# Performance work log

Hardware: AMD Instinct MI355X
Metric: run time of the kernel (lower is better)

The kernel has to match this reference:

```python
import jax, jax.numpy as jnp
import numpy as np
import math

B, N, T, H, HEADS, FIN, NL_TR = 4, 256, 16, 128, 4, 2, 5
M = B * N
NEG = -1e9

def _sinusoidal(t, h):
    pos = jnp.arange(t, dtype=jnp.float32)[:, None]
    div = jnp.exp(jnp.arange(0, h, 2, dtype=jnp.float32) * (-math.log(10000.0) / h))
    pe = jnp.zeros((t, h), dtype=jnp.float32)
    pe = pe.at[:, 0::2].set(jnp.sin(pos * div))
    pe = pe.at[:, 1::2].set(jnp.cos(pos * div))
    return pe

def _gat(x, W, a_src, a_dst, b, E, m):
    # x: [T,M,F]; W: [F,heads,H]; E: [T,M,M] bool, E[t,i,j]=edge j->i; m: [T,M] bool
    h = jnp.einsum('tmf,fhd->tmhd', x, W)
    ss = jnp.einsum('tmhd,hd->tmh', h, a_src)  # source score per node
    sd = jnp.einsum('tmhd,hd->tmh', h, a_dst)  # dest score per node
    logits = jax.nn.leaky_relu(sd[:, :, None, :] + ss[:, None, :, :], 0.2)  # [T,i,j,h]
    logits = jnp.where(E[..., None], logits, NEG)
    alpha = jax.nn.softmax(logits, axis=2)  # segment-softmax over incoming edges
    out = jnp.einsum('tijh,tjhd->tihd', alpha, h).mean(axis=2) + b  # concat=False -> head mean + bias
    return jax.nn.relu(out) * m[..., None]

def _ln(x, s, b):
    mu = x.mean(-1, keepdims=True)
    v = ((x - mu) ** 2).mean(-1, keepdims=True)
    return (x - mu) / jnp.sqrt(v + 1e-5) * s + b

def _forward(ego_mask, positions, adjacency, gat1_W, gat1_asrc, gat1_adst, gat1_b, gatW, gat_asrc, gat_adst, gat_b, Wqkv, bqkv, Wo, bo, ln1_s, ln1_b, ln2_s, ln2_b, Wff1, bff1, Wff2, bff2):
    m = jnp.transpose(ego_mask, (1, 0, 2)).reshape(T, M)  # [T, B*N]
    eye = jnp.eye(M, dtype=bool)
    # edge j->i valid iff A[t,j,i]!=0 and both nodes masked; PyG GATConv adds self-loops
    E = ((jnp.swapaxes(adjacency, 1, 2) != 0) & m[:, :, None] & m[:, None, :]) | (eye[None] & m[:, :, None])
    x = _gat(positions, gat1_W, gat1_asrc, gat1_adst, gat1_b, E, m)
    for i in range(5):
        x = _gat(x, gatW[i], gat_asrc[i], gat_adst[i], gat_b[i], E, m)
    x_seq = jnp.transpose(x, (1, 0, 2)) + _sinusoidal(T, H)[None]  # [M, T, H]
    dh = H // HEADS
    scale = 1.0 / math.sqrt(dh)
    for l in range(NL_TR):
        q = (x_seq @ Wqkv[l, 0] + bqkv[l, 0]).reshape(M, T, HEADS, dh)
        k = (x_seq @ Wqkv[l, 1] + bqkv[l, 1]).reshape(M, T, HEADS, dh)
        v = (x_seq @ Wqkv[l, 2] + bqkv[l, 2]).reshape(M, T, HEADS, dh)
        sc = jnp.einsum('bqhd,bkhd->bhqk', q, k) * scale
        a = jax.nn.softmax(sc, axis=-1)
        o = jnp.einsum('bhqk,bkhd->bqhd', a, v).reshape(M, T, H) @ Wo[l] + bo[l]
        x_seq = _ln(x_seq + o, ln1_s[l], ln1_b[l])
        f = jax.nn.relu(x_seq @ Wff1[l] + bff1[l]) @ Wff2[l] + bff2[l]
        x_seq = _ln(x_seq + f, ln2_s[l], ln2_b[l])
    return x_seq.reshape(B, N, T, H)

def setup_inputs() -> dict:
    key = jax.random.key(0)
    ks = jax.random.split(key, 32)
    s = 0.05
    f32 = jnp.float32
    inp = {
        'ego_mask': jax.random.uniform(ks[0], (B, T, N)) < 0.95,
        'positions': jax.random.normal(ks[1], (T, M, FIN), dtype=f32),
        'adjacency': (jax.random.uniform(ks[2], (T, M, M)) < 0.02).astype(f32),
        'gat1_W': jax.random.normal(ks[3], (FIN, HEADS, H), dtype=f32) * s,
        'gat1_asrc': jax.random.normal(ks[4], (HEADS, H), dtype=f32) * s,
        'gat1_adst': jax.random.normal(ks[5], (HEADS, H), dtype=f32) * s,
        'gat1_b': jnp.zeros((H,), dtype=f32),
        'gatW': jax.random.normal(ks[6], (5, H, HEADS, H), dtype=f32) * s,
        'gat_asrc': jax.random.normal(ks[7], (5, HEADS, H), dtype=f32) * s,
        'gat_adst': jax.random.normal(ks[8], (5, HEADS, H), dtype=f32) * s,
        'gat_b': jnp.zeros((5, H), dtype=f32),
        'Wqkv': jax.random.normal(ks[9], (NL_TR, 3, H, H), dtype=f32) * s,
        'bqkv': jnp.zeros((NL_TR, 3, H), dtype=f32),
        'Wo': jax.random.normal(ks[10], (NL_TR, H, H), dtype=f32) * s,
        'bo': jnp.zeros((NL_TR, H), dtype=f32),
        'ln1_s': jnp.ones((NL_TR, H), dtype=f32),
        'ln1_b': jnp.zeros((NL_TR, H), dtype=f32),
        'ln2_s': jnp.ones((NL_TR, H), dtype=f32),
        'ln2_b': jnp.zeros((NL_TR, H), dtype=f32),
        'Wff1': jax.random.normal(ks[11], (NL_TR, H, 4 * H), dtype=f32) * s,
        'bff1': jnp.zeros((NL_TR, 4 * H), dtype=f32),
        'Wff2': jax.random.normal(ks[12], (NL_TR, 4 * H, H), dtype=f32) * s,
        'bff2': jnp.zeros((NL_TR, H), dtype=f32),
    }
    return inp

def reference(ego_mask, positions, adjacency, gat1_W, gat1_asrc, gat1_adst, gat1_b, gatW, gat_asrc, gat_adst, gat_b, Wqkv, bqkv, Wo, bo, ln1_s, ln1_b, ln2_s, ln2_b, Wff1, bff1, Wff2, bff2):
    return _forward(ego_mask, positions, adjacency, gat1_W, gat1_asrc, gat1_adst, gat1_b, gatW, gat_asrc, gat_adst, gat_b, Wqkv, bqkv, Wo, bo, ln1_s, ln1_b, ln2_s, ln2_b, Wff1, bff1, Wff2, bff2)
```

## Files before the change

### kernel.cpp

```cpp
#include <hip/hip_runtime.h>
#include <hip/hip_bf16.h>

#define TT 16
#define MM 1024
#define HDIM 128
#define NHEADS 4
#define NROWS (TT*MM)
#define MAXDEG 64

typedef __bf16 bf16x8 __attribute__((ext_vector_type(8)));
typedef float f32x4 __attribute__((ext_vector_type(4)));

__device__ __forceinline__ unsigned short f2b(float x) {
    unsigned u = __float_as_uint(x);
    u += 0x7fff + ((u >> 16) & 1);
    return (unsigned short)(u >> 16);
}
__device__ __forceinline__ float bu2f(unsigned short u) {
    return __uint_as_float(((unsigned)u) << 16);
}

__global__ __launch_bounds__(256) void k_init(const int* __restrict__ ego,
                                              float* __restrict__ mfl,
                                              int* __restrict__ cnt) {
    int idx = blockIdx.x * 256 + threadIdx.x;
    int t = idx >> 10, i = idx & 1023;
    int b = i >> 8, n = i & 255;
    mfl[idx] = ego[b * (TT * 256) + t * 256 + n] ? 1.f : 0.f;
    cnt[idx] = 0;
}

__global__ __launch_bounds__(256) void k_edges(const float* __restrict__ adj,
                                               const float* __restrict__ mfl,
                                               int* __restrict__ cnt,
                                               int* __restrict__ nbr) {
    int bid = blockIdx.x;
    int t = bid >> 6, jc = bid & 63;
    int tid = threadIdx.x;
    int i0 = tid * 4;
    int rowb = t * MM;
    float mi[4];
#pragma unroll
    for (int r = 0; r < 4; ++r) mi[r] = mfl[rowb + i0 + r];
    __shared__ float ms[16];
    if (tid < 16) ms[tid] = mfl[rowb + jc * 16 + tid];
    __syncthreads();
    const float* at = adj + (size_t)t * MM * MM;
#pragma unroll 4
    for (int jj = 0; jj < 16; ++jj) {
        int j = jc * 16 + jj;
        float4 a = *(const float4*)(at + (size_t)j * MM + i0);
        float mj = ms[jj];
#pragma unroll
        for (int r = 0; r < 4; ++r) {
            int i = i0 + r;
            bool e;
            if (j == i) e = (mi[r] != 0.f);
            else e = ((&a.x)[r] != 0.f) && (mj != 0.f) && (mi[r] != 0.f);
            if (e) {
                int row = rowb + i;
                int pos = atomicAdd(&cnt[row], 1);
                if (pos < MAXDEG) nbr[(size_t)row * MAXDEG + pos] = j;
            }
        }
    }
}

__global__ __launch_bounds__(256) void k_prep(const float* __restrict__ Wqkv,
                                              const float* __restrict__ Wo,
                                              const float* __restrict__ Wff1,
                                              const float* __restrict__ Wff2,
                                              const float* __restrict__ gW,
                                              unsigned short* __restrict__ Wb) {
    int o = blockIdx.x * 256 + threadIdx.x;
    const float* src; int cs;
    if (o < 122880) {
        int l = o / 24576, r = o % 24576;
        if (r < 6144) {
            int nt = r >> 8, rem = r & 255, ks = rem >> 6, lane = rem & 63;
            int mt = nt >> 3, cc = nt & 7;
            int k = ks * 32 + ((lane >> 4) << 3), c = cc * 16 + (lane & 15);
            src = Wqkv + ((size_t)(l * 3 + mt) * 128 + k) * 128 + c; cs = 128;
        } else if (r < 8192) {
            int u = r - 6144, nt = u >> 8, rem = u & 255, ks = rem >> 6, lane = rem & 63;
            int k = ks * 32 + ((lane >> 4) << 3), c = nt * 16 + (lane & 15);
            src = Wo + (size_t)l * 16384 + (size_t)k * 128 + c; cs = 128;
        } else if (r < 16384) {
            int u = r - 8192, nt = u >> 8, rem = u & 255, ks = rem >> 6, lane = rem & 63;
            int k = ks * 32 + ((lane >> 4) << 3), c = nt * 16 + (lane & 15);
            src = Wff1 + (size_t)l * 65536 + (size_t)k * 512 + c; cs = 512;
        } else {
            int u = r - 16384, nt = u >> 10, rem = u & 1023, ks = rem >> 6, lane = rem & 63;
            int k = ks * 32 + ((lane >> 4) << 3), c = nt * 16 + (lane & 15);
            src = Wff2 + (size_t)l * 65536 + (size_t)k * 128 + c; cs = 128;
        }
    } else {
        int u = o - 122880;
        int l = u >> 13, rr = u & 8191;
        int nt = rr >> 8, rem = rr & 255, ks = rem >> 6, lane = rem & 63;
        int k = ks * 32 + ((lane >> 4) << 3), c = nt * 16 + (lane & 15);
        src = gW + (size_t)l * 65536 + (size_t)k * 512 + c; cs = 512;
    }
    unsigned v[4];
#pragma unroll
    for (int j = 0; j < 4; ++j)
        v[j] = (unsigned)f2b(src[(2 * j) * (size_t)cs]) |
               ((unsigned)f2b(src[(2 * j + 1) * (size_t)cs]) << 16);
    *(uint4*)(Wb + (size_t)o * 8) = make_uint4(v[0], v[1], v[2], v[3]);
}

__global__ __launch_bounds__(128) void k_gat1(const float* __restrict__ x,
                                              const float* __restrict__ W,
                                              const float* __restrict__ asrc,
                                              const float* __restrict__ adst,
                                              unsigned short* __restrict__ h16,
                                              float* __restrict__ ss,
                                              float* __restrict__ sd) {
    int bid = blockIdx.x;
    int row = ((bid & 7) << 11) + (bid >> 3);
    int tid = threadIdx.x;
    float x0 = x[row * 2], x1 = x[row * 2 + 1];
    float s4[4], d4[4];
#pragma unroll
    for (int hh = 0; hh < 4; ++hh) {
        int o = hh * 128 + tid;
        float v = x0 * W[o] + x1 * W[512 + o];
        h16[(size_t)row * 512 + o] = f2b(v);
        s4[hh] = v * asrc[o];
        d4[hh] = v * adst[o];
    }
#pragma unroll
    for (int hh = 0; hh < 4; ++hh)
        for (int off = 32; off; off >>= 1) {
            s4[hh] += __shfl_down(s4[hh], off, 64);
            d4[hh] += __shfl_down(d4[hh], off, 64);
        }
    __shared__ float red[2][2][4];
    if ((tid & 63) == 0) {
        int w = tid >> 6;
#pragma unroll
        for (int hh = 0; hh < 4; ++hh) { red[w][0][hh] = s4[hh]; red[w][1][hh] = d4[hh]; }
    }
    __syncthreads();
    if (tid < 4) ss[row * 4 + tid] = red[0][0][tid] + red[1][0][tid];
    else if (tid < 8) sd[row * 4 + tid - 4] = red[0][1][tid - 4] + red[1][1][tid - 4];
}

__global__ __launch_bounds__(256, 2) void k_gat_h(const unsigned short* __restrict__ x16,
                                                  const unsigned short* __restrict__ Wg,
                                                  const float* __restrict__ asrc,
                                                  const float* __restrict__ adst,
                                                  unsigned short* __restrict__ h16,
                                                  float* __restrict__ ss,
                                                  float* __restrict__ sd) {
    __shared__ __align__(16) unsigned short xb[32 * 136];
    int bid = blockIdx.x;
    int row0 = (((bid & 7) << 6) + (bid >> 3)) * 32;
    int tid = threadIdx.x;
#pragma unroll
    for (int q = 0; q < 2; ++q) {
        int u = tid + q * 256;
        int rr = u >> 4, cc = (u & 15) * 8;
        *(uint4*)(xb + rr * 136 + cc) = *(const uint4*)(x16 + (size_t)(row0 + rr) * 128 + cc);
    }
    __syncthreads();
    const int lane = tid & 63, w = tid >> 6;
    const int mrow = lane & 15, quad = lane >> 4;
    float ps[2][4] = {{0,0,0,0},{0,0,0,0}}, pd[2][4] = {{0,0,0,0},{0,0,0,0}};
#pragma unroll
    for (int ib = 0; ib < 4; ++ib) {
        bf16x8 wb[8];
#pragma unroll
        for (int u = 0; u < 2; ++u) {
            int nt = w * 8 + ib * 2 + u;
#pragma unroll
            for (int ks = 0; ks < 4; ++ks)
                wb[u * 4 + ks] = *(const bf16x8*)(Wg + (size_t)((nt * 4 + ks) * 64 + lane) * 8);
        }
#pragma unroll
        for (int rg = 0; rg < 2; ++rg) {
            bf16x8 af[4];
#pragma unroll
            for (int ks = 0; ks < 4; ++ks)
                af[ks] = *(const bf16x8*)(xb + (rg * 16 + mrow) * 136 + ks * 32 + quad * 8);
            f32x4 acc[2];
            acc[0] = (f32x4){0.f, 0.f, 0.f, 0.f};
            acc[1] = (f32x4){0.f, 0.f, 0.f, 0.f};
#pragma unroll
            for (int u = 0; u < 2; ++u)
#pragma unroll
                for (int ks = 0; ks < 4; ++ks)
                    acc[u] = __builtin_amdgcn_mfma_f32_16x16x32_bf16(af[ks], wb[u * 4 + ks], acc[u], 0, 0, 0);
#pragma unroll
            for (int u = 0; u < 2; ++u) {
                int nt = w * 8 + ib * 2 + u, col = nt * 16 + mrow;
                float as_ = asrc[col], ad_ = adst[col];
#pragma unroll
                for (int r = 0; r < 4; ++r) {
                    float v = acc[u][r];
                    h16[(size_t)(row0 + rg * 16 + quad * 4 + r) * 512 + col] = f2b(v);
                    ps[rg][r] += v * as_; pd[rg][r] += v * ad_;
                }
            }
        }
    }
#pragma unroll
    for (int off = 1; off < 16; off <<= 1)
#pragma unroll
        for (int rg = 0; rg < 2; ++rg)
#pragma unroll
            for (int r = 0; r < 4; ++r) {
                ps[rg][r] += __shfl_xor(ps[rg][r], off, 64);
                pd[rg][r] += __shfl_xor(pd[rg][r], off, 64);
            }
    if (mrow == 0) {
#pragma unroll
        for (int rg = 0; rg < 2; ++rg)
#pragma unroll
            for (int r = 0; r < 4; ++r) {
                int row = row0 + rg * 16 + quad * 4 + r;
                ss[row * 4 + w] = ps[rg][r];
                sd[row * 4 + w] = pd[rg][r];
            }
    }
}

__global__ __launch_bounds__(256, 2) void k_agg(const unsigned short* __restrict__ h16,
                                                const float* __restrict__ ss,
                                                const float* __restrict__ sd,
                                                const int* __restrict__ cnt,
                                                const int* __restrict__ nbr,
                                                const float* __restrict__ mfl,
                                                const float* __restrict__ bias,
                                                unsigned short* __restrict__ xo16) {
    __shared__ float alB[4][MAXDEG][4];
    __shared__ int   nbB[4][MAXDEG];
    __shared__ __align__(16) float partB[4][512];
    int bid = blockIdx.x;
    int row0 = (((bid & 7) << 9) + (bid >> 3)) * 4;
    int tid = threadIdx.x;
    const int w = tid >> 6, lane = tid & 63;
    int row = row0 + w, t = row >> 10;
    bool valid = mfl[row] != 0.f;
    int c = 0;
    if (valid) { c = cnt[row]; if (c > MAXDEG) c = MAXDEG; }
    bool act = lane < c;
    int jreg = 0;
    float lg[4];
    if (act) {
        jreg = nbr[(size_t)row * MAXDEG + lane];
        int jr = t * MM + jreg;
#pragma unroll
        for (int hh = 0; hh < 4; ++hh) {
            float v = sd[row * 4 + hh] + ss[jr * 4 + hh];
            lg[hh] = v > 0.f ? v : 0.2f * v;
        }
    } else {
#pragma unroll
        for (int hh = 0; hh < 4; ++hh) lg[hh] = -1e30f;
    }
    float mx[4];
#pragma unroll
    for (int hh = 0; hh < 4; ++hh) mx[hh] = lg[hh];
#pragma unroll
    for (int off = 32; off; off >>= 1)
#pragma unroll
        for (int hh = 0; hh < 4; ++hh) mx[hh] = fmaxf(mx[hh], __shfl_xor(mx[hh], off, 64));
    float ev[4];
#pragma unroll
    for (int hh = 0; hh < 4; ++hh) ev[hh] = act ? __expf(lg[hh] - mx[hh]) : 0.f;
    float sm[4];
#pragma unroll
    for (int hh = 0; hh < 4; ++hh) sm[hh] = ev[hh];
#pragma unroll
    for (int off = 32; off; off >>= 1)
#pragma unroll
        for (int hh = 0; hh < 4; ++hh) sm[hh] += __shfl_xor(sm[hh], off, 64);
    if (act) {
        float4 a4 = make_float4(ev[0] / sm[0], ev[1] / sm[1], ev[2] / sm[2], ev[3] / sm[3]);
        *(float4*)&alB[w][lane][0] = a4;
        nbB[w][lane] = jreg;
    }
    __syncthreads();
    const int head = lane >> 4;
    float acc[8] = {0, 0, 0, 0, 0, 0, 0, 0};
    const unsigned short* hb = h16 + (size_t)t * MM * 512 + lane * 8;
    for (int n = 0; n < c; ++n) {
        int j = nbB[w][n];
        float a = alB[w][n][head];
        uint4 v = *(const uint4*)(hb + (size_t)j * 512);
        acc[0] += a * bu2f((unsigned short)(v.x & 0xffff));
        acc[1] += a * bu2f((unsigned short)(v.x >> 16));
        acc[2] += a * bu2f((unsigned short)(v.y & 0xffff));
        acc[3] += a * bu2f((unsigned short)(v.y >> 16));
        acc[4] += a * bu2f((unsigned short)(v.z & 0xffff));
        acc[5] += a * bu2f((unsigned short)(v.z >> 16));
        acc[6] += a * bu2f((unsigned short)(v.w & 0xffff));
        acc[7] += a * bu2f((unsigned short)(v.w >> 16));
    }
    *(float4*)&partB[w][lane * 8]     = make_float4(acc[0], acc[1], acc[2], acc[3]);
    *(float4*)&partB[w][lane * 8 + 4] = make_float4(acc[4], acc[5], acc[6], acc[7]);
    __syncthreads();
    {
        int d0 = lane * 2;
        unsigned outp = 0;
#pragma unroll
        for (int q = 0; q < 2; ++q) {
            int d = d0 + q;
            float v = 0.f;
            if (valid) {
                v = 0.25f * (partB[w][d] + partB[w][128 + d] + partB[w][256 + d] + partB[w][384 + d])
                    + bias[d];
                v = fmaxf(v, 0.f);
            }
            outp |= ((unsigned)f2b(v)) << (16 * q);
        }
        *(unsigned*)(xo16 + (size_t)row * 128 + d0) = outp;
    }
}

__device__ __forceinline__ void ln256(float* xs, const float* s, const float* b) {
    int tid = threadIdx.x, row = tid >> 4, lane = tid & 15;
    float* xr = xs + row * 128;
    float sum = 0.f;
#pragma unroll
    for (int k2 = 0; k2 < 8; ++k2) sum += xr[lane + 16 * k2];
#pragma unroll
    for (int off = 8; off; off >>= 1) sum += __shfl_xor(sum, off, 16);
    float mean = sum * (1.f / 128.f);
    float vs = 0.f;
#pragma unroll
    for (int k2 = 0; k2 < 8; ++k2) { float d = xr[lane + 16 * k2] - mean; vs += d * d; }
#pragma unroll
    for (int off = 8; off; off >>= 1) vs += __shfl_xor(vs, off, 16);
    float rstd = rsqrtf(vs * (1.f / 128.f) + 1e-5f);
#pragma unroll
    for (int k2 = 0; k2 < 8; ++k2) {
        int d = lane + 16 * k2;
        float v = (xr[d] - mean) * rstd;
        xr[d] = v * s[d] + b[d];
    }
    __syncthreads();
}

__global__ __launch_bounds__(256, 2) void k_tf(const unsigned short* __restrict__ xg,
        const unsigned short* __restrict__ Wb,
        const float* __restrict__ bqkv, const float* __restrict__ bo,
        const float* __restrict__ ln1s, const float* __restrict__ ln1b,
        const float* __restrict__ ln2s, const float* __restrict__ ln2b,
        const float* __restrict__ bff1, const float* __restrict__ bff2,
        float* __restrict__ out) {
    __shared__ __align__(16) float smem[8320];
    float* xs = smem;
    float* sb = smem + 2048;
    unsigned short* xb16  = (unsigned short*)(smem + 3072);
    unsigned short* Qb16  = (unsigned short*)(smem + 4160);
    unsigned short* Kb16  = (unsigned short*)(smem + 5248);
    unsigned short* Vb16  = (unsigned short*)(smem + 6336);
    unsigned short* hid16 = (unsigned short*)(smem + 4160);
    const int m = blockIdx.x, tid = threadIdx.x;
    const int lane = tid & 63, w = tid >> 6;
    const int mrow = lane & 15, quad = lane >> 4;

    for (int idx = tid; idx < 2048; idx += 256) {
        int t = idx >> 7, d = idx & 127, jj = d >> 1;
        float arg = (float)t * expf(-(float)(2 * jj) * (9.210340371976184f / 128.f));
        float pe = (d & 1) ? cosf(arg) : sinf(arg);
        xs[idx] = bu2f(xg[(size_t)t * (MM * HDIM) + (size_t)m * HDIM + d]) + pe;
    }
    __syncthreads();

    const int crow = tid >> 4, ccb = (tid & 15) * 8;
    for (int l = 0; l < 5; ++l) {
        const unsigned short* Wl = Wb + (size_t)l * 196608;
        {
            const float* xp = xs + crow * 128 + ccb;
            unsigned v[4];
#pragma unroll
            for (int j = 0; j < 4; ++j)
                v[j] = (unsigned)f2b(xp[2 * j]) | ((unsigned)f2b(xp[2 * j + 1]) << 16);
            *(uint4*)(xb16 + crow * 136 + ccb) = make_uint4(v[0], v[1], v[2], v[3]);
        }
        __syncthreads();
        {
            bf16x8 af[4];
#pragma unroll
            for (int ks = 0; ks < 4; ++ks)
                af[ks] = *(const bf16x8*)(xb16 + mrow * 136 + ks * 32 + quad * 8);
            f32x4 acc[6];
#pragma unroll
            for (int i = 0; i < 6; ++i) acc[i] = (f32x4){0.f, 0.f, 0.f, 0.f};
#pragma unroll
            for (int ib = 0; ib < 3; ++ib) {
                bf16x8 wb[8];
#pragma unroll
                for (int u = 0; u < 2; ++u) {
                    int nt = w * 6 + ib * 2 + u;
                    const unsigned short* bp = Wl + (size_t)(nt * 4) * 512 + lane * 8;
#pragma unroll
                    for (int ks = 0; ks < 4; ++ks)
                        wb[u * 4 + ks] = *(const bf16x8*)(bp + ks * 512);
                }
#pragma unroll
                for (int u = 0; u < 2; ++u)
#pragma unroll
                    for (int ks = 0; ks < 4; ++ks)
                        acc[ib * 2 + u] = __builtin_amdgcn_mfma_f32_16x16x32_bf16(af[ks], wb[u * 4 + ks], acc[ib * 2 + u], 0, 0, 0);
            }
#pragma unroll
            for (int i = 0; i < 6; ++i) {
                int nt = w * 6 + i, mt = nt >> 3, cc = nt & 7;
                int col = cc * 16 + mrow;
                float bb = bqkv[l * 384 + mt * 128 + col];
                unsigned short* dst = (mt == 0) ? Qb16 : (mt == 1) ? Kb16 : Vb16;
#pragma unroll
                for (int r = 0; r < 4; ++r)
                    dst[(quad * 4 + r) * 136 + col] = f2b(acc[i][r] + bb);
            }
        }
        __syncthreads();
        {
            int hh = tid >> 6, tq = (tid >> 2) & 15, tk0 = (tid & 3) * 4;
            const unsigned short* qp = Qb16 + tq * 136 + hh * 32;
            float a[4] = {0.f, 0.f, 0.f, 0.f};
#pragma unroll
            for (int d4 = 0; d4 < 4; ++d4) {
                uint4 qv = *(const uint4*)(qp + d4 * 8);
                float qf[8];
                qf[0] = bu2f((unsigned short)(qv.x & 0xffff)); qf[1] = bu2f((unsigned short)(qv.x >> 16));
                qf[2] = bu2f((unsigned short)(qv.y & 0xffff)); qf[3] = bu2f((unsigned short)(qv.y >> 16));
                qf[4] = bu2f((unsigned short)(qv.z & 0xffff)); qf[5] = bu2f((unsigned short)(qv.z >> 16));
                qf[6] = bu2f((unsigned short)(qv.w & 0xffff)); qf[7] = bu2f((unsigned short)(qv.w >> 16));
#pragma unroll
                for (int j = 0; j < 4; ++j) {
                    uint4 kv = *(const uint4*)(Kb16 + (tk0 + j) * 136 + hh * 32 + d4 * 8);
                    a[j] += qf[0] * bu2f((unsigned short)(kv.x & 0xffff));
                    a[j] += qf[1] * bu2f((unsigned short)(kv.x >> 16));
                    a[j] += qf[2] * bu2f((unsigned short)(kv.y & 0xffff));
                    a[j] += qf[3] * bu2f((unsigned short)(kv.y >> 16));
                    a[j] += qf[4] * bu2f((unsigned short)(kv.z & 0xffff));
                    a[j] += qf[5] * bu2f((unsigned short)(kv.z >> 16));
                    a[j] += qf[6] * bu2f((unsigned short)(kv.w & 0xffff));
                    a[j] += qf[7] * bu2f((unsigned short)(kv.w >> 16));
                }
            }
#pragma unroll
            for (int j = 0; j < 4; ++j)
                sb[(tk0 + j) * 64 + hh * 16 + tq] = a[j] * 0.17677669529663687f;
        }
        __syncthreads();
        if (tid < 64) {
            float mx = -1e30f;
#pragma unroll
            for (int u = 0; u < 16; ++u) mx = fmaxf(mx, sb[u * 64 + tid]);
            float s = 0.f;
#pragma unroll
            for (int u = 0; u < 16; ++u) { float e = __expf(sb[u * 64 + tid] - mx); sb[u * 64 + tid] = e; s += e; }
            float inv = 1.f / s;
#pragma unroll
            for (int u = 0; u < 16; ++u) sb[u * 64 + tid] *= inv;
        }
        __syncthreads();
        {
            int o = tid & 127, r0p = (tid >> 7) * 8, hh = o >> 5;
            float accp[8] = {0, 0, 0, 0, 0, 0, 0, 0};
            for (int u = 0; u < 16; ++u) {
                float vv = bu2f(Vb16[u * 136 + o]);
                const float* pp = sb + u * 64 + hh * 16 + r0p;
#pragma unroll
                for (int r = 0; r < 8; ++r) accp[r] += pp[r] * vv;
            }
#pragma unroll
            for (int r = 0; r < 8; ++r)
                xb16[(r0p + r) * 136 + o] = f2b(accp[r]);
        }
        __syncthreads();
        {
            bf16x8 af[4];
#pragma unroll
            for (int ks = 0; ks < 4; ++ks)
                af[ks] = *(const bf16x8*)(xb16 + mrow * 136 + ks * 32 + quad * 8);
            const unsigned short* Ws = Wl + 49152;
            bf16x8 wb[8];
#pragma unroll
            for (int u = 0; u < 2; ++u) {
                int nt = w * 2 + u;
#pragma unroll
                for (int ks = 0; ks < 4; ++ks)
                    wb[u * 4 + ks] = *(const bf16x8*)(Ws + (size_t)((nt * 4 + ks) * 64 + lane) * 8);
            }
            f32x4 acc[2];
            acc[0] = (f32x4){0.f, 0.f, 0.f, 0.f};
            acc[1] = (f32x4){0.f, 0.f, 0.f, 0.f};
#pragma unroll
            for (int u = 0; u < 2; ++u)
#pragma unroll
                for (int ks = 0; ks < 4; ++ks)
                    acc[u] = __builtin_amdgcn_mfma_f32_16x16x32_bf16(af[ks], wb[u * 4 + ks], acc[u], 0, 0, 0);
#pragma unroll
            for (int u = 0; u < 2; ++u) {
                int col = (w * 2 + u) * 16 + mrow;
                float bb = bo[l * 128 + col];
#pragma unroll
                for (int r = 0; r < 4; ++r)
                    xs[(quad * 4 + r) * 128 + col] += acc[u][r] + bb;
            }
        }
        __syncthreads();
        ln256(xs, ln1s + l * 128, ln1b + l * 128);
        {
            const float* xp = xs + crow * 128 + ccb;
            unsigned v[4];
#pragma unroll
            for (int j = 0; j < 4; ++j)
                v[j] = (unsigned)f2b(xp[2 * j]) | ((unsigned)f2b(xp[2 * j + 1]) << 16);
            *(uint4*)(xb16 + crow * 136 + ccb) = make_uint4(v[0], v[1], v[2], v[3]);
        }
        __syncthreads();
        {
            bf16x8 af[4];
#pragma unroll
            for (int ks = 0; ks < 4; ++ks)
                af[ks] = *(const bf16x8*)(xb16 + mrow * 136 + ks * 32 + quad * 8);
            f32x4 acc[8];
#pragma unroll
            for (int i = 0; i < 8; ++i) acc[i] = (f32x4){0.f, 0.f, 0.f, 0.f};
            const unsigned short* Ws = Wl + 65536;
#pragma unroll
            for (int ib = 0; ib < 4; ++ib) {
                bf16x8 wb[8];
#pragma unroll
                for (int u = 0; u < 2; ++u) {
                    int nt = w * 8 + ib * 2 + u;
#pragma unroll
                    for (int ks = 0; ks < 4; ++ks)
                        wb[u * 4 + ks] = *(const bf16x8*)(Ws + (size_t)((nt * 4 + ks) * 64 + lane) * 8);
                }
#pragma unroll
                for (int u = 0; u < 2; ++u)
#pragma unroll
                    for (int ks = 0; ks < 4; ++ks)
                        acc[ib * 2 + u] = __builtin_amdgcn_mfma_f32_16x16x32_bf16(af[ks], wb[u * 4 + ks], acc[ib * 2 + u], 0, 0, 0);
            }
#pragma unroll
            for (int i = 0; i < 8; ++i) {
                int col = (w * 8 + i) * 16 + mrow;
                float bb = bff1[l * 512 + col];
#pragma unroll
                for (int r = 0; r < 4; ++r) {
                    float v = fmaxf(acc[i][r] + bb, 0.f);
                    hid16[(quad * 4 + r) * 520 + col] = f2b(v);
                }
            }
        }
        __syncthreads();
        {
            f32x4 a0 = (f32x4){0.f, 0.f, 0.f, 0.f};
            f32x4 a1 = (f32x4){0.f, 0.f, 0.f, 0.f};
            const unsigned short* Ws = Wl + 131072;
            int nt0 = w * 2, nt1 = w * 2 + 1;
#pragma unroll
            for (int kb = 0; kb < 4; ++kb) {
                bf16x8 afb[4], w0[4], w1[4];
#pragma unroll
                for (int kk = 0; kk < 4; ++kk) {
                    int ks = kb * 4 + kk;
                    afb[kk] = *(const bf16x8*)(hid16 + mrow * 520 + ks * 32 + quad * 8);
                    w0[kk] = *(const bf16x8*)(Ws + (size_t)((nt0 * 16 + ks) * 64 + lane) * 8);
                    w1[kk] = *(const bf16x8*)(Ws + (size_t)((nt1 * 16 + ks) * 64 + lane) * 8);
                }
#pragma unroll
                for (int kk = 0; kk < 4; ++kk) {
                    a0 = __builtin_amdgcn_mfma_f32_16x16x32_bf16(afb[kk], w0[kk], a0, 0, 0, 0);
                    a1 = __builtin_amdgcn_mfma_f32_16x16x32_bf16(afb[kk], w1[kk], a1, 0, 0, 0);
                }
            }
            int col0 = nt0 * 16 + mrow, col1 = nt1 * 16 + mrow;
            float bb0 = bff2[l * 128 + col0], bb1 = bff2[l * 128 + col1];
#pragma unroll
            for (int r = 0; r < 4; ++r) {
                xs[(quad * 4 + r) * 128 + col0] += a0[r] + bb0;
                xs[(quad * 4 + r) * 128 + col1] += a1[r] + bb1;
            }
        }
        __syncthreads();
        ln256(xs, ln2s + l * 128, ln2b + l * 128);
    }
    for (int idx = tid; idx < 2048; idx += 256)
        out[(size_t)m * 2048 + idx] = xs[idx];
}

extern "C" void kernel_launch(void* const* d_in, const int* in_sizes, int n_in,
                              void* d_out, int out_size, void* d_ws, size_t ws_size,
                              hipStream_t stream) {
    (void)in_sizes; (void)n_in; (void)out_size; (void)ws_size;
    const int*   ego  = (const int*)d_in[0];
    const float* pos  = (const float*)d_in[1];
    const float* adj  = (const float*)d_in[2];
    const float* g1W  = (const float*)d_in[3];
    const float* g1as = (const float*)d_in[4];
    const float* g1ad = (const float*)d_in[5];
    const float* g1b  = (const float*)d_in[6];
    const float* gW   = (const float*)d_in[7];
    const float* gas  = (const float*)d_in[8];
    const float* gad  = (const float*)d_in[9];
    const float* gb   = (const float*)d_in[10];
    const float* Wqkv = (const float*)d_in[11];
    const float* bqkv = (const float*)d_in[12];
    const float* Wo   = (const float*)d_in[13];
    const float* bo   = (const float*)d_in[14];
    const float* l1s  = (const float*)d_in[15];
    const float* l1b  = (const float*)d_in[16];
    const float* l2s  = (const float*)d_in[17];
    const float* l2b  = (const float*)d_in[18];
    const float* Wff1 = (const float*)d_in[19];
    const float* bff1 = (const float*)d_in[20];
    const float* Wff2 = (const float*)d_in[21];
    const float* bff2 = (const float*)d_in[22];

    unsigned short* x0  = (unsigned short*)d_ws;
    unsigned short* x1  = x0 + 2097152;
    unsigned short* h16 = x1 + 2097152;
    float* ssb = (float*)(h16 + 8388608);
    float* sdb = ssb + 65536;
    float* mfl = sdb + 65536;
    int*   cnt = (int*)(mfl + 16384);
    int*   nbr = cnt + 16384;
    unsigned short* Wb16 = (unsigned short*)(nbr + 1048576);
    unsigned short* Wg16 = Wb16 + 983040;

    k_prep<<<640, 256, 0, stream>>>(Wqkv, Wo, Wff1, Wff2, gW, Wb16);
    k_init<<<64, 256, 0, stream>>>(ego, mfl, cnt);
    k_edges<<<1024, 256, 0, stream>>>(adj, mfl, cnt, nbr);

    k_gat1<<<NROWS, 128, 0, stream>>>(pos, g1W, g1as, g1ad, h16, ssb, sdb);
    k_agg<<<4096, 256, 0, stream>>>(h16, ssb, sdb, cnt, nbr, mfl, g1b, x0);

    unsigned short* xin = x0; unsigned short* xout = x1;
    for (int L = 0; L < 5; ++L) {
        k_gat_h<<<512, 256, 0, stream>>>(xin, Wg16 + (size_t)L * 65536,
                                         gas + L * 512, gad + L * 512, h16, ssb, sdb);
        k_agg<<<4096, 256, 0, stream>>>(h16, ssb, sdb, cnt, nbr, mfl, gb + L * 128, xout);
        unsigned short* tmp = xin; xin = xout; xout = tmp;
    }

    k_tf<<<MM, 256, 0, stream>>>(xin, Wb16, bqkv, bo, l1s, l1b, l2s, l2b,
                                 bff1, bff2, (float*)d_out);
}
```

Before: 511.6 us.

## Process two sequences per transformer block with 512 threads and fused LN-to-bf16

The transformer kernel now handles two sequences per block with 512 threads, so each group of four waves works on its own sequence while the block shares barriers and global weight fetches. Accumulator arrays are cut from 6/8 tiles to 2 live tiles per inner iteration, which lowers register pressure so the raised launch bounds can be met. LayerNorm now writes the bf16 copy directly, removing a separate conversion pass and one barrier per sublayer. Shared memory per block roughly doubles, which may limit how many blocks fit on a CU.

```diff
diff --git a/kernel.cpp b/kernel.cpp
--- a/kernel.cpp
+++ b/kernel.cpp
@@ -319,7 +319,8 @@
     }
 }
 
-__device__ __forceinline__ void ln256(float* xs, const float* s, const float* b) {
+__device__ __forceinline__ void ln512(float* xs, unsigned short* xbB,
+                                      const float* s, const float* b) {
     int tid = threadIdx.x, row = tid >> 4, lane = tid & 15;
     float* xr = xs + row * 128;
     float sum = 0.f;
@@ -337,90 +338,96 @@
 #pragma unroll
     for (int k2 = 0; k2 < 8; ++k2) {
         int d = lane + 16 * k2;
-        float v = (xr[d] - mean) * rstd;
-        xr[d] = v * s[d] + b[d];
-    }
-    __syncthreads();
-}
-
-__global__ __launch_bounds__(256, 2) void k_tf(const unsigned short* __restrict__ xg,
+        float v = (xr[d] - mean) * rstd * s[d] + b[d];
+        xr[d] = v;
+        xbB[row * 136 + d] = f2b(v);
+    }
+    __syncthreads();
+}
+
+__global__ __launch_bounds__(512, 4) void k_tf(const unsigned short* __restrict__ xg,
         const unsigned short* __restrict__ Wb,
         const float* __restrict__ bqkv, const float* __restrict__ bo,
         const float* __restrict__ ln1s, const float* __restrict__ ln1b,
         const float* __restrict__ ln2s, const float* __restrict__ ln2b,
         const float* __restrict__ bff1, const float* __restrict__ bff2,
         float* __restrict__ out) {
-    __shared__ __align__(16) float smem[8320];
-    float* xs = smem;
-    float* sb = smem + 2048;
-    unsigned short* xb16  = (unsigned short*)(smem + 3072);
-    unsigned short* Qb16  = (unsigned short*)(smem + 4160);
-    unsigned short* Kb16  = (unsigned short*)(smem + 5248);
-    unsigned short* Vb16  = (unsigned short*)(smem + 6336);
-    unsigned short* hid16 = (unsigned short*)(smem + 4160);
-    const int m = blockIdx.x, tid = threadIdx.x;
+    __shared__ __align__(16) float smem[16640];
+    float* xs  = smem;
+    float* sbB = smem + 4096;
+    unsigned short* xbB  = (unsigned short*)(smem + 6144);
+    unsigned short* qkvB = (unsigned short*)(smem + 8320);
+    const int m0 = blockIdx.x * 2, tid = threadIdx.x;
     const int lane = tid & 63, w = tid >> 6;
+    const int sid = w >> 2, w4 = w & 3;
     const int mrow = lane & 15, quad = lane >> 4;
-
-    for (int idx = tid; idx < 2048; idx += 256) {
-        int t = idx >> 7, d = idx & 127, jj = d >> 1;
+    unsigned short* xb16  = xbB + sid * 2176;
+    unsigned short* Qb16  = qkvB + sid * 8320;
+    unsigned short* Kb16  = Qb16 + 2176;
+    unsigned short* Vb16  = Qb16 + 4352;
+    unsigned short* hid16 = Qb16;
+    float* sb  = sbB + sid * 1024;
+    float* xss = xs + sid * 2048;
+
+    for (int idx = tid; idx < 4096; idx += 512) {
+        int sq = idx >> 11, t = (idx >> 7) & 15, d = idx & 127, jj = d >> 1;
         float arg = (float)t * expf(-(float)(2 * jj) * (9.210340371976184f / 128.f));
         float pe = (d & 1) ? cosf(arg) : sinf(arg);
-        xs[idx] = bu2f(xg[(size_t)t * (MM * HDIM) + (size_t)m * HDIM + d]) + pe;
-    }
-    __syncthreads();
-
-    const int crow = tid >> 4, ccb = (tid & 15) * 8;
+        xs[idx] = bu2f(xg[(size_t)t * (MM * HDIM) + (size_t)(m0 + sq) * HDIM + d]) + pe;
+    }
+    __syncthreads();
+    {
+        const int crow = tid >> 4, ccb = (tid & 15) * 8;
+        const float* xp = xs + crow * 128 + ccb;
+        unsigned v[4];
+#pragma unroll
+        for (int j = 0; j < 4; ++j)
+            v[j] = (unsigned)f2b(xp[2 * j]) | ((unsigned)f2b(xp[2 * j + 1]) << 16);
+        *(uint4*)(xbB + crow * 136 + ccb) = make_uint4(v[0], v[1], v[2], v[3]);
+    }
+    __syncthreads();
+
     for (int l = 0; l < 5; ++l) {
         const unsigned short* Wl = Wb + (size_t)l * 196608;
         {
-            const float* xp = xs + crow * 128 + ccb;
-            unsigned v[4];
-#pragma unroll
-            for (int j = 0; j < 4; ++j)
-                v[j] = (unsigned)f2b(xp[2 * j]) | ((unsigned)f2b(xp[2 * j + 1]) << 16);
-            *(uint4*)(xb16 + crow * 136 + ccb) = make_uint4(v[0], v[1], v[2], v[3]);
+            bf16x8 af[4];
+#pragma unroll
+            for (int ks = 0; ks < 4; ++ks)
+                af[ks] = *(const bf16x8*)(xb16 + mrow * 136 + ks * 32 + quad * 8);
+#pragma unroll
+            for (int ib = 0; ib < 3; ++ib) {
+                bf16x8 wb[8];
+#pragma unroll
+                for (int u = 0; u < 2; ++u) {
+                    int nt = w4 * 6 + ib * 2 + u;
+                    const unsigned short* bp = Wl + (size_t)(nt * 4) * 512 + lane * 8;
+#pragma unroll
+                    for (int ks = 0; ks < 4; ++ks)
+                        wb[u * 4 + ks] = *(const bf16x8*)(bp + ks * 512);
+                }
+                f32x4 acc[2];
+                acc[0] = (f32x4){0.f, 0.f, 0.f, 0.f};
+                acc[1] = (f32x4){0.f, 0.f, 0.f, 0.f};
+#pragma unroll
+                for (int u = 0; u < 2; ++u)
+#pragma unroll
+                    for (int ks = 0; ks < 4; ++ks)
+                        acc[u] = __builtin_amdgcn_mfma_f32_16x16x32_bf16(af[ks], wb[u * 4 + ks], acc[u], 0, 0, 0);
+#pragma unroll
+                for (int u = 0; u < 2; ++u) {
+                    int nt = w4 * 6 + ib * 2 + u, mt = nt >> 3, cc = nt & 7;
+                    int col = cc * 16 + mrow;
+                    float bb = bqkv[l * 384 + mt * 128 + col];
+                    unsigned short* dst = (mt == 0) ? Qb16 : (mt == 1) ? Kb16 : Vb16;
+#pragma unroll
+                    for (int r = 0; r < 4; ++r)
+                        dst[(quad * 4 + r) * 136 + col] = f2b(acc[u][r] + bb);
+                }
+            }
         }
         __syncthreads();
         {
-            bf16x8 af[4];
-#pragma unroll
-            for (int ks = 0; ks < 4; ++ks)
-                af[ks] = *(const bf16x8*)(xb16 + mrow * 136 + ks * 32 + quad * 8);
-            f32x4 acc[6];
-#pragma unroll
-            for (int i = 0; i < 6; ++i) acc[i] = (f32x4){0.f, 0.f, 0.f, 0.f};
-#pragma unroll
-            for (int ib = 0; ib < 3; ++ib) {
-                bf16x8 wb[8];
-#pragma unroll
-                for (int u = 0; u < 2; ++u) {
-                    int nt = w * 6 + ib * 2 + u;
-                    const unsigned short* bp = Wl + (size_t)(nt * 4) * 512 + lane * 8;
-#pragma unroll
-                    for (int ks = 0; ks < 4; ++ks)
-                        wb[u * 4 + ks] = *(const bf16x8*)(bp + ks * 512);
-                }
-#pragma unroll
-                for (int u = 0; u < 2; ++u)
-#pragma unroll
-                    for (int ks = 0; ks < 4; ++ks)
-                        acc[ib * 2 + u] = __builtin_amdgcn_mfma_f32_16x16x32_bf16(af[ks], wb[u * 4 + ks], acc[ib * 2 + u], 0, 0, 0);
-            }
-#pragma unroll
-            for (int i = 0; i < 6; ++i) {
-                int nt = w * 6 + i, mt = nt >> 3, cc = nt & 7;
-                int col = cc * 16 + mrow;
-                float bb = bqkv[l * 384 + mt * 128 + col];
-                unsigned short* dst = (mt == 0) ? Qb16 : (mt == 1) ? Kb16 : Vb16;
-#pragma unroll
-                for (int r = 0; r < 4; ++r)
-                    dst[(quad * 4 + r) * 136 + col] = f2b(acc[i][r] + bb);
-            }
-        }
-        __syncthreads();
-        {
-            int hh = tid >> 6, tq = (tid >> 2) & 15, tk0 = (tid & 3) * 4;
+            int hh = w4, tq = (tid >> 2) & 15, tk0 = (tid & 3) * 4;
             const unsigned short* qp = Qb16 + tq * 136 + hh * 32;
             float a[4] = {0.f, 0.f, 0.f, 0.f};
 #pragma unroll
@@ -449,20 +456,22 @@
                 sb[(tk0 + j) * 64 + hh * 16 + tq] = a[j] * 0.17677669529663687f;
         }
         __syncthreads();
-        if (tid < 64) {
+        if (tid < 128) {
+            float* sbp = sbB + (tid >> 6) * 1024;
+            int cc = tid & 63;
             float mx = -1e30f;
 #pragma unroll
-            for (int u = 0; u < 16; ++u) mx = fmaxf(mx, sb[u * 64 + tid]);
+            for (int u = 0; u < 16; ++u) mx = fmaxf(mx, sbp[u * 64 + cc]);
             float s = 0.f;
 #pragma unroll
-            for (int u = 0; u < 16; ++u) { float e = __expf(sb[u * 64 + tid] - mx); sb[u * 64 + tid] = e; s += e; }
+            for (int u = 0; u < 16; ++u) { float e = __expf(sbp[u * 64 + cc] - mx); sbp[u * 64 + cc] = e; s += e; }
             float inv = 1.f / s;
 #pragma unroll
-            for (int u = 0; u < 16; ++u) sb[u * 64 + tid] *= inv;
+            for (int u = 0; u < 16; ++u) sbp[u * 64 + cc] *= inv;
         }
         __syncthreads();
         {
-            int o = tid & 127, r0p = (tid >> 7) * 8, hh = o >> 5;
+            int o = tid & 127, r0p = ((tid >> 7) & 1) * 8, hh = o >> 5;
             float accp[8] = {0, 0, 0, 0, 0, 0, 0, 0};
             for (int u = 0; u < 16; ++u) {
                 float vv = bu2f(Vb16[u * 136 + o]);
@@ -484,7 +493,7 @@
             bf16x8 wb[8];
 #pragma unroll
             for (int u = 0; u < 2; ++u) {
-                int nt = w * 2 + u;
+                int nt = w4 * 2 + u;
 #pragma unroll
                 for (int ks = 0; ks < 4; ++ks)
                     wb[u * 4 + ks] = *(const bf16x8*)(Ws + (size_t)((nt * 4 + ks) * 64 + lane) * 8);
@@ -499,57 +508,48 @@
                     acc[u] = __builtin_amdgcn_mfma_f32_16x16x32_bf16(af[ks], wb[u * 4 + ks], acc[u], 0, 0, 0);
 #pragma unroll
             for (int u = 0; u < 2; ++u) {
-                int col = (w * 2 + u) * 16 + mrow;
+                int col = (w4 * 2 + u) * 16 + mrow;
                 float bb = bo[l * 128 + col];
 #pragma unroll
                 for (int r = 0; r < 4; ++r)
-                    xs[(quad * 4 + r) * 128 + col] += acc[u][r] + bb;
+                    xss[(quad * 4 + r) * 128 + col] += acc[u][r] + bb;
             }
         }
         __syncthreads();
-        ln256(xs, ln1s + l * 128, ln1b + l * 128);
-        {
-            const float* xp = xs + crow * 128 + ccb;
-            unsigned v[4];
-#pragma unroll
-            for (int j = 0; j < 4; ++j)
-                v[j] = (unsigned)f2b(xp[2 * j]) | ((unsigned)f2b(xp[2 * j + 1]) << 16);
-            *(uint4*)(xb16 + crow * 136 + ccb) = make_uint4(v[0], v[1], v[2], v[3]);
-        }
-        __syncthreads();
+        ln512(xs, xbB, ln1s + l * 128, ln1b + l * 128);
         {
             bf16x8 af[4];
 #pragma unroll
             for (int ks = 0; ks < 4; ++ks)
                 af[ks] = *(const bf16x8*)(xb16 + mrow * 136 + ks * 32 + quad * 8);
-            f32x4 acc[8];
-#pragma unroll
-            for (int i = 0; i < 8; ++i) acc[i] = (f32x4){0.f, 0.f, 0.f, 0.f};
             const unsigned short* Ws = Wl + 65536;
 #pragma unroll
             for (int ib = 0; ib < 4; ++ib) {
                 bf16x8 wb[8];
 #pragma unroll
                 for (int u = 0; u < 2; ++u) {
-                    int nt = w * 8 + ib * 2 + u;
+                    int nt = w4 * 8 + ib * 2 + u;
 #pragma unroll
                     for (int ks = 0; ks < 4; ++ks)
                         wb[u * 4 + ks] = *(const bf16x8*)(Ws + (size_t)((nt * 4 + ks) * 64 + lane) * 8);
                 }
+                f32x4 acc[2];
+                acc[0] = (f32x4){0.f, 0.f, 0.f, 0.f};
+                acc[1] = (f32x4){0.f, 0.f, 0.f, 0.f};
 #pragma unroll
                 for (int u = 0; u < 2; ++u)
 #pragma unroll
                     for (int ks = 0; ks < 4; ++ks)
-                        acc[ib * 2 + u] = __builtin_amdgcn_mfma_f32_16x16x32_bf16(af[ks], wb[u * 4 + ks], acc[ib * 2 + u], 0, 0, 0);
-            }
-#pragma unroll
-            for (int i = 0; i < 8; ++i) {
-                int col = (w * 8 + i) * 16 + mrow;
-                float bb = bff1[l * 512 + col];
-#pragma unroll
-                for (int r = 0; r < 4; ++r) {
-                    float v = fmaxf(acc[i][r] + bb, 0.f);
-                    hid16[(quad * 4 + r) * 520 + col] = f2b(v);
+                        acc[u] = __builtin_amdgcn_mfma_f32_16x16x32_bf16(af[ks], wb[u * 4 + ks], acc[u], 0, 0, 0);
+#pragma unroll
+                for (int u = 0; u < 2; ++u) {
+                    int col = (w4 * 8 + ib * 2 + u) * 16 + mrow;
+                    float bb = bff1[l * 512 + col];
+#pragma unroll
+                    for (int r = 0; r < 4; ++r) {
+                        float v = fmaxf(acc[u][r] + bb, 0.f);
+                        hid16[(quad * 4 + r) * 520 + col] = f2b(v);
+                    }
                 }
             }
         }
@@ -558,7 +558,7 @@
             f32x4 a0 = (f32x4){0.f, 0.f, 0.f, 0.f};
             f32x4 a1 = (f32x4){0.f, 0.f, 0.f, 0.f};
             const unsigned short* Ws = Wl + 131072;
-            int nt0 = w * 2, nt1 = w * 2 + 1;
+            int nt0 = w4 * 2, nt1 = w4 * 2 + 1;
 #pragma unroll
             for (int kb = 0; kb < 4; ++kb) {
                 bf16x8 afb[4], w0[4], w1[4];
@@ -579,15 +579,15 @@
             float bb0 = bff2[l * 128 + col0], bb1 = bff2[l * 128 + col1];
 #pragma unroll
             for (int r = 0; r < 4; ++r) {
-                xs[(quad * 4 + r) * 128 + col0] += a0[r] + bb0;
-                xs[(quad * 4 + r) * 128 + col1] += a1[r] + bb1;
+                xss[(quad * 4 + r) * 128 + col0] += a0[r] + bb0;
+                xss[(quad * 4 + r) * 128 + col1] += a1[r] + bb1;
             }
         }
         __syncthreads();
-        ln256(xs, ln2s + l * 128, ln2b + l * 128);
-    }
-    for (int idx = tid; idx < 2048; idx += 256)
-        out[(size_t)m * 2048 + idx] = xs[idx];
+        ln512(xs, xbB, ln2s + l * 128, ln2b + l * 128);
+    }
+    for (int idx = tid; idx < 4096; idx += 512)
+        out[(size_t)m0 * 2048 + idx] = xs[idx];
 }
 
 extern "C" void kernel_launch(void* const* d_in, const int* in_sizes, int n_in,
@@ -644,6 +644,6 @@
         unsigned short* tmp = xin; xin = xout; xout = tmp;
     }
 
-    k_tf<<<MM, 256, 0, stream>>>(xin, Wb16, bqkv, bo, l1s, l1b, l2s, l2b,
-                                 bff1, bff2, (float*)d_out);
-}
+    k_tf<<<512, 512, 0, stream>>>(xin, Wb16, bqkv, bo, l1s, l1b, l2s, l2b,
+                                  bff1, bff2, (float*)d_out);
+}
```

Result: slower. 543.1 us (+6.1%).

## Move transformer attention onto MFMA and fuse bf16 conversion into layernorm

Applied to the files above, without the earlier changes.

Per-head QK^T and PV in the transformer kernel now use MFMA bf16 16x16x32 instructions, one wave per head. The softmax is done in registers with cross-lane shuffles, replacing the scalar dot-product loops and the separate softmax and PV passes through shared memory. V is stored transposed, and probabilities go to a small per-wave LDS buffer with the K dimension zero-padded from 16 to 32. Layernorm now also writes the bf16 copy of x, which removes separate conversion passes and barriers. Accumulators are scoped per ib block to cut register pressure, and shared memory shrinks slightly, trading some extra precision loss from rounding P to bf16.

```diff
diff --git a/kernel.cpp b/kernel.cpp
--- a/kernel.cpp
+++ b/kernel.cpp
@@ -18,6 +18,12 @@
 }
 __device__ __forceinline__ float bu2f(unsigned short u) {
     return __uint_as_float(((unsigned)u) << 16);
+}
+__device__ __forceinline__ bf16x8 bzero8() {
+    bf16x8 z;
+#pragma unroll
+    for (int j = 0; j < 8; ++j) z[j] = (__bf16)0.0f;
+    return z;
 }
 
 __global__ __launch_bounds__(256) void k_init(const int* __restrict__ ego,
@@ -319,7 +325,8 @@
     }
 }
 
-__device__ __forceinline__ void ln256(float* xs, const float* s, const float* b) {
+__device__ __forceinline__ void ln256(float* xs, unsigned short* xb,
+                                      const float* s, const float* b) {
     int tid = threadIdx.x, row = tid >> 4, lane = tid & 15;
     float* xr = xs + row * 128;
     float sum = 0.f;
@@ -337,8 +344,9 @@
 #pragma unroll
     for (int k2 = 0; k2 < 8; ++k2) {
         int d = lane + 16 * k2;
-        float v = (xr[d] - mean) * rstd;
-        xr[d] = v * s[d] + b[d];
+        float v = (xr[d] - mean) * rstd * s[d] + b[d];
+        xr[d] = v;
+        xb[row * 136 + d] = f2b(v);
     }
     __syncthreads();
 }
@@ -350,14 +358,14 @@
         const float* __restrict__ ln2s, const float* __restrict__ ln2b,
         const float* __restrict__ bff1, const float* __restrict__ bff2,
         float* __restrict__ out) {
-    __shared__ __align__(16) float smem[8320];
+    __shared__ __align__(16) float smem[7616];
     float* xs = smem;
-    float* sb = smem + 2048;
-    unsigned short* xb16  = (unsigned short*)(smem + 3072);
-    unsigned short* Qb16  = (unsigned short*)(smem + 4160);
-    unsigned short* Kb16  = (unsigned short*)(smem + 5248);
-    unsigned short* Vb16  = (unsigned short*)(smem + 6336);
-    unsigned short* hid16 = (unsigned short*)(smem + 4160);
+    unsigned short* xb16  = (unsigned short*)(smem + 2048);
+    unsigned short* Qb16  = (unsigned short*)(smem + 3136);
+    unsigned short* Kb16  = Qb16 + 2176;
+    unsigned short* Vt16  = Kb16 + 2176;
+    unsigned short* Pl16  = Vt16 + 3072;
+    unsigned short* hid16 = Qb16;
     const int m = blockIdx.x, tid = threadIdx.x;
     const int lane = tid & 63, w = tid >> 6;
     const int mrow = lane & 15, quad = lane >> 4;
@@ -369,27 +377,24 @@
         xs[idx] = bu2f(xg[(size_t)t * (MM * HDIM) + (size_t)m * HDIM + d]) + pe;
     }
     __syncthreads();
-
-    const int crow = tid >> 4, ccb = (tid & 15) * 8;
+    {
+        const int crow = tid >> 4, ccb = (tid & 15) * 8;
+        const float* xp = xs + crow * 128 + ccb;
+        unsigned v[4];
+#pragma unroll
+        for (int j = 0; j < 4; ++j)
+            v[j] = (unsigned)f2b(xp[2 * j]) | ((unsigned)f2b(xp[2 * j + 1]) << 16);
+        *(uint4*)(xb16 + crow * 136 + ccb) = make_uint4(v[0], v[1], v[2], v[3]);
+    }
+    __syncthreads();
+
     for (int l = 0; l < 5; ++l) {
         const unsigned short* Wl = Wb + (size_t)l * 196608;
         {
-            const float* xp = xs + crow * 128 + ccb;
-            unsigned v[4];
-#pragma unroll
-            for (int j = 0; j < 4; ++j)
-                v[j] = (unsigned)f2b(xp[2 * j]) | ((unsigned)f2b(xp[2 * j + 1]) << 16);
-            *(uint4*)(xb16 + crow * 136 + ccb) = make_uint4(v[0], v[1], v[2], v[3]);
-        }
-        __syncthreads();
-        {
             bf16x8 af[4];
 #pragma unroll
             for (int ks = 0; ks < 4; ++ks)
                 af[ks] = *(const bf16x8*)(xb16 + mrow * 136 + ks * 32 + quad * 8);
-            f32x4 acc[6];
-#pragma unroll
-            for (int i = 0; i < 6; ++i) acc[i] = (f32x4){0.f, 0.f, 0.f, 0.f};
 #pragma unroll
             for (int ib = 0; ib < 3; ++ib) {
                 bf16x8 wb[8];
@@ -401,78 +406,68 @@
                     for (int ks = 0; ks < 4; ++ks)
                         wb[u * 4 + ks] = *(const bf16x8*)(bp + ks * 512);
                 }
+                f32x4 acc[2];
+                acc[0] = (f32x4){0.f, 0.f, 0.f, 0.f};
+                acc[1] = (f32x4){0.f, 0.f, 0.f, 0.f};
 #pragma unroll
                 for (int u = 0; u < 2; ++u)
 #pragma unroll
                     for (int ks = 0; ks < 4; ++ks)
-                        acc[ib * 2 + u] = __builtin_amdgcn_mfma_f32_16x16x32_bf16(af[ks], wb[u * 4 + ks], acc[ib * 2 + u], 0, 0, 0);
-            }
-#pragma unroll
-            for (int i = 0; i < 6; ++i) {
-                int nt = w * 6 + i, mt = nt >> 3, cc = nt & 7;
-                int col = cc * 16 + mrow;
-                float bb = bqkv[l * 384 + mt * 128 + col];
-                unsigned short* dst = (mt == 0) ? Qb16 : (mt == 1) ? Kb16 : Vb16;
-#pragma unroll
-                for (int r = 0; r < 4; ++r)
-                    dst[(quad * 4 + r) * 136 + col] = f2b(acc[i][r] + bb);
+                        acc[u] = __builtin_amdgcn_mfma_f32_16x16x32_bf16(af[ks], wb[u * 4 + ks], acc[u], 0, 0, 0);
+#pragma unroll
+                for (int u = 0; u < 2; ++u) {
+                    int nt = w * 6 + ib * 2 + u, mt = nt >> 3, cc = nt & 7;
+                    int col = cc * 16 + mrow;
+                    float bb = bqkv[l * 384 + mt * 128 + col];
+                    if (mt == 2) {
+#pragma unroll
+                        for (int r = 0; r < 4; ++r)
+                            Vt16[col * 24 + quad * 4 + r] = f2b(acc[u][r] + bb);
+                    } else {
+                        unsigned short* dst = (mt == 0) ? Qb16 : Kb16;
+#pragma unroll
+                        for (int r = 0; r < 4; ++r)
+                            dst[(quad * 4 + r) * 136 + col] = f2b(acc[u][r] + bb);
+                    }
+                }
             }
         }
         __syncthreads();
         {
-            int hh = tid >> 6, tq = (tid >> 2) & 15, tk0 = (tid & 3) * 4;
-            const unsigned short* qp = Qb16 + tq * 136 + hh * 32;
-            float a[4] = {0.f, 0.f, 0.f, 0.f};
-#pragma unroll
-            for (int d4 = 0; d4 < 4; ++d4) {
-                uint4 qv = *(const uint4*)(qp + d4 * 8);
-                float qf[8];
-                qf[0] = bu2f((unsigned short)(qv.x & 0xffff)); qf[1] = bu2f((unsigned short)(qv.x >> 16));
-                qf[2] = bu2f((unsigned short)(qv.y & 0xffff)); qf[3] = bu2f((unsigned short)(qv.y >> 16));
-                qf[4] = bu2f((unsigned short)(qv.z & 0xffff)); qf[5] = bu2f((unsigned short)(qv.z >> 16));
-                qf[6] = bu2f((unsigned short)(qv.w & 0xffff)); qf[7] = bu2f((unsigned short)(qv.w >> 16));
-#pragma unroll
-                for (int j = 0; j < 4; ++j) {
-                    uint4 kv = *(const uint4*)(Kb16 + (tk0 + j) * 136 + hh * 32 + d4 * 8);
-                    a[j] += qf[0] * bu2f((unsigned short)(kv.x & 0xffff));
-                    a[j] += qf[1] * bu2f((unsigned short)(kv.x >> 16));
-                    a[j] += qf[2] * bu2f((unsigned short)(kv.y & 0xffff));
-                    a[j] += qf[3] * bu2f((unsigned short)(kv.y >> 16));
-                    a[j] += qf[4] * bu2f((unsigned short)(kv.z & 0xffff));
-                    a[j] += qf[5] * bu2f((unsigned short)(kv.z >> 16));
-                    a[j] += qf[6] * bu2f((unsigned short)(kv.w & 0xffff));
-                    a[j] += qf[7] * bu2f((unsigned short)(kv.w >> 16));
-                }
-            }
-#pragma unroll
-            for (int j = 0; j < 4; ++j)
-                sb[(tk0 + j) * 64 + hh * 16 + tq] = a[j] * 0.17677669529663687f;
-        }
-        __syncthreads();
-        if (tid < 64) {
-            float mx = -1e30f;
-#pragma unroll
-            for (int u = 0; u < 16; ++u) mx = fmaxf(mx, sb[u * 64 + tid]);
-            float s = 0.f;
-#pragma unroll
-            for (int u = 0; u < 16; ++u) { float e = __expf(sb[u * 64 + tid] - mx); sb[u * 64 + tid] = e; s += e; }
-            float inv = 1.f / s;
-#pragma unroll
-            for (int u = 0; u < 16; ++u) sb[u * 64 + tid] *= inv;
-        }
-        __syncthreads();
-        {
-            int o = tid & 127, r0p = (tid >> 7) * 8, hh = o >> 5;
-            float accp[8] = {0, 0, 0, 0, 0, 0, 0, 0};
-            for (int u = 0; u < 16; ++u) {
-                float vv = bu2f(Vb16[u * 136 + o]);
-                const float* pp = sb + u * 64 + hh * 16 + r0p;
-#pragma unroll
-                for (int r = 0; r < 8; ++r) accp[r] += pp[r] * vv;
-            }
-#pragma unroll
-            for (int r = 0; r < 8; ++r)
-                xb16[(r0p + r) * 136 + o] = f2b(accp[r]);
+            const int hb = w * 32;
+            bf16x8 qa = *(const bf16x8*)(Qb16 + mrow * 136 + hb + quad * 8);
+            bf16x8 ka = *(const bf16x8*)(Kb16 + mrow * 136 + hb + quad * 8);
+            f32x4 sc = (f32x4){0.f, 0.f, 0.f, 0.f};
+            sc = __builtin_amdgcn_mfma_f32_16x16x32_bf16(qa, ka, sc, 0, 0, 0);
+            float p[4], mx0[4], sm0[4];
+#pragma unroll
+            for (int r = 0; r < 4; ++r) { p[r] = sc[r] * 0.17677669529663687f; mx0[r] = p[r]; }
+#pragma unroll
+            for (int off = 1; off < 16; off <<= 1)
+#pragma unroll
+                for (int r = 0; r < 4; ++r) mx0[r] = fmaxf(mx0[r], __shfl_xor(mx0[r], off, 64));
+#pragma unroll
+            for (int r = 0; r < 4; ++r) { p[r] = __expf(p[r] - mx0[r]); sm0[r] = p[r]; }
+#pragma unroll
+            for (int off = 1; off < 16; off <<= 1)
+#pragma unroll
+                for (int r = 0; r < 4; ++r) sm0[r] += __shfl_xor(sm0[r], off, 64);
+            unsigned short* Pw = Pl16 + w * 384;
+#pragma unroll
+            for (int r = 0; r < 4; ++r)
+                Pw[(quad * 4 + r) * 24 + mrow] = f2b(p[r] / sm0[r]);
+            bf16x8 pa = (quad < 2) ? *(const bf16x8*)(Pw + mrow * 24 + quad * 8) : bzero8();
+#pragma unroll
+            for (int half = 0; half < 2; ++half) {
+                int dbase = hb + half * 16;
+                bf16x8 vb = (quad < 2) ? *(const bf16x8*)(Vt16 + (dbase + mrow) * 24 + quad * 8)
+                                       : bzero8();
+                f32x4 oc = (f32x4){0.f, 0.f, 0.f, 0.f};
+                oc = __builtin_amdgcn_mfma_f32_16x16x32_bf16(pa, vb, oc, 0, 0, 0);
+#pragma unroll
+                for (int r = 0; r < 4; ++r)
+                    xb16[(quad * 4 + r) * 136 + dbase + mrow] = f2b(oc[r]);
+            }
         }
         __syncthreads();
         {
@@ -507,24 +502,12 @@
             }
         }
         __syncthreads();
-        ln256(xs, ln1s + l * 128, ln1b + l * 128);
-        {
-            const float* xp = xs + crow * 128 + ccb;
-            unsigned v[4];
-#pragma unroll
-            for (int j = 0; j < 4; ++j)
-                v[j] = (unsigned)f2b(xp[2 * j]) | ((unsigned)f2b(xp[2 * j + 1]) << 16);
-            *(uint4*)(xb16 + crow * 136 + ccb) = make_uint4(v[0], v[1], v[2], v[3]);
-        }
-        __syncthreads();
+        ln256(xs, xb16, ln1s + l * 128, ln1b + l * 128);
         {
             bf16x8 af[4];
 #pragma unroll
             for (int ks = 0; ks < 4; ++ks)
                 af[ks] = *(const bf16x8*)(xb16 + mrow * 136 + ks * 32 + quad * 8);
-            f32x4 acc[8];
-#pragma unroll
-            for (int i = 0; i < 8; ++i) acc[i] = (f32x4){0.f, 0.f, 0.f, 0.f};
             const unsigned short* Ws = Wl + 65536;
 #pragma unroll
             for (int ib = 0; ib < 4; ++ib) {
@@ -536,20 +519,23 @@
                     for (int ks = 0; ks < 4; ++ks)
                         wb[u * 4 + ks] = *(const bf16x8*)(Ws + (size_t)((nt * 4 + ks) * 64 + lane) * 8);
                 }
+                f32x4 acc[2];
+                acc[0] = (f32x4){0.f, 0.f, 0.f, 0.f};
+                acc[1] = (f32x4){0.f, 0.f, 0.f, 0.f};
 #pragma unroll
                 for (int u = 0; u < 2; ++u)
 #pragma unroll
                     for (int ks = 0; ks < 4; ++ks)
-                        acc[ib * 2 + u] = __builtin_amdgcn_mfma_f32_16x16x32_bf16(af[ks], wb[u * 4 + ks], acc[ib * 2 + u], 0, 0, 0);
-            }
-#pragma unroll
-            for (int i = 0; i < 8; ++i) {
-                int col = (w * 8 + i) * 16 + mrow;
-                float bb = bff1[l * 512 + col];
-#pragma unroll
-                for (int r = 0; r < 4; ++r) {
-                    float v = fmaxf(acc[i][r] + bb, 0.f);
-                    hid16[(quad * 4 + r) * 520 + col] = f2b(v);
+                        acc[u] = __builtin_amdgcn_mfma_f32_16x16x32_bf16(af[ks], wb[u * 4 + ks], acc[u], 0, 0, 0);
+#pragma unroll
+                for (int u = 0; u < 2; ++u) {
+                    int col = (w * 8 + ib * 2 + u) * 16 + mrow;
+                    float bb = bff1[l * 512 + col];
+#pragma unroll
+                    for (int r = 0; r < 4; ++r) {
+                        float v = fmaxf(acc[u][r] + bb, 0.f);
+                        hid16[(quad * 4 + r) * 520 + col] = f2b(v);
+                    }
                 }
             }
         }
@@ -584,7 +570,7 @@
             }
         }
         __syncthreads();
-        ln256(xs, ln2s + l * 128, ln2b + l * 128);
+        ln256(xs, xb16, ln2s + l * 128, ln2b + l * 128);
     }
     for (int idx = tid; idx < 2048; idx += 256)
         out[(size_t)m * 2048 + idx] = xs[idx];
```

Result: slower. 547.3 us (+7.0%).
